# Kernel tuning notes

Hardware: AMD Instinct MI355X
Metric: run time of the kernel (lower is better)

The kernel has to match this reference:

```python
import jax, jax.numpy as jnp
import numpy as np

B, L, D, H = 4, 1024, 1024, 16
HD = D // H          # head dim = 64
NUM_CASES = 8        # Sanskrit vibhakti cases
SCALE = float(np.sqrt(HD))


def setup_inputs() -> dict:
    key = jax.random.key(0)
    ks = jax.random.split(key, 13)
    s = 0.02
    return {
        "x": jax.random.normal(ks[0], (B, L, D), jnp.float32),
        "case_ids": jax.random.randint(ks[1], (B, L), 0, NUM_CASES, jnp.int32),
        "verb_mask": jax.random.randint(ks[2], (B, L), 0, 2, jnp.int32),
        "Wq": jax.random.normal(ks[3], (D, D), jnp.float32) * s,
        "bq": jnp.zeros((D,), jnp.float32),
        "Wk": jax.random.normal(ks[4], (D, D), jnp.float32) * s,
        "bk": jnp.zeros((D,), jnp.float32),
        "Wv": jax.random.normal(ks[5], (D, D), jnp.float32) * s,
        "bv": jnp.zeros((D,), jnp.float32),
        "Wo": jax.random.normal(ks[6], (D, D), jnp.float32) * s,
        "bo": jnp.zeros((D,), jnp.float32),
        "case_bias": jax.random.normal(ks[7], (H, NUM_CASES, NUM_CASES), jnp.float32) * s,
        "verb_bias": jax.random.normal(ks[8], (H,), jnp.float32) * s,
    }


def reference(x, case_ids, verb_mask, Wq, bq, Wk, bk, Wv, bv, Wo, bo, case_bias, verb_bias):
    b, l, d = x.shape

    def split_heads(t):  # [B,L,D] -> [B,H,L,HD]
        return t.reshape(b, l, H, HD).transpose(0, 2, 1, 3)

    Q = split_heads(x @ Wq + bq)
    K = split_heads(x @ Wk + bk)
    V = split_heads(x @ Wv + bv)

    scores = jnp.einsum('bhid,bhjd->bhij', Q, K) / SCALE  # [B,H,L,L]

    # Panini constraint bias: per-head case-pair bias + per-head verb-position bias
    cb = case_bias[:, case_ids[:, :, None], case_ids[:, None, :]]  # [H,B,L,L]
    cb = cb.transpose(1, 0, 2, 3)                                  # [B,H,L,L]
    vb = verb_bias[None, :, None, None] * verb_mask[:, None, None, :].astype(scores.dtype)
    scores = scores + cb + vb

    weights = jax.nn.softmax(scores, axis=-1)  # dropout is identity in eval
    out = jnp.einsum('bhij,bhjd->bhid', weights, V)       # [B,H,L,HD]
    out = out.transpose(0, 2, 1, 3).reshape(b, l, d)
    return out @ Wo + bo
```

## Files before the change

kernel.cpp:

```cpp
#include <hip/hip_runtime.h>

#define BB 4
#define LL 1024
#define DD 1024
#define HH 16
#define HDD 64

typedef __bf16 bf16x8 __attribute__((ext_vector_type(8)));
typedef float f32x4 __attribute__((ext_vector_type(4)));
typedef float f32x16 __attribute__((ext_vector_type(16)));
typedef unsigned short u16x8 __attribute__((ext_vector_type(8)));
typedef unsigned short u16x4 __attribute__((ext_vector_type(4)));
typedef unsigned int u32x4v __attribute__((ext_vector_type(4)));
typedef unsigned int u32x2 __attribute__((ext_vector_type(2)));

#define LOG2E 1.4426950408889634f

__device__ __forceinline__ unsigned short f2bf(float f) {
    unsigned int u = __builtin_bit_cast(unsigned int, f);
    u += 0x7FFFu + ((u >> 16) & 1u);
    return (unsigned short)(u >> 16);
}

__device__ __forceinline__ unsigned int cvtpk_bf16(float lo, float hi) {
    unsigned int r;
    asm("v_cvt_pk_bf16_f32 %0, %1, %2" : "=v"(r) : "v"(lo), "v"(hi));
    return r;
}

__global__ __launch_bounds__(256) void cvt_x(const float* __restrict__ x,
                                             unsigned short* __restrict__ xb) {
    const int i = (blockIdx.x * 256 + threadIdx.x) * 8;
    f32x4 a0 = *(const f32x4*)(x + i);
    f32x4 a1 = *(const f32x4*)(x + i + 4);
    u16x8 o;
#pragma unroll
    for (int j = 0; j < 4; ++j) { o[j] = f2bf(a0[j]); o[4 + j] = f2bf(a1[j]); }
    *(u16x8*)(xb + i) = o;
}

__global__ __launch_bounds__(256) void trans_w(const float* __restrict__ Wq,
                                               const float* __restrict__ Wk,
                                               const float* __restrict__ Wv,
                                               const float* __restrict__ Wo,
                                               unsigned short* __restrict__ Wqkv_t,
                                               unsigned short* __restrict__ Wo_t) {
    __shared__ unsigned short lds[64 * 72];
    const int t = threadIdx.x;
    const int mat = blockIdx.z;
    const float* W = (mat == 0) ? Wq : (mat == 1) ? Wk : (mat == 2) ? Wv : Wo;
    unsigned short* out = (mat < 3) ? (Wqkv_t + (size_t)mat * 1024 * 1024) : Wo_t;
    const int k0 = blockIdx.x * 64;
    const int n0 = blockIdx.y * 64;
#pragma unroll
    for (int p = 0; p < 4; ++p) {
        int c = t + p * 256;
        int kr = c >> 4, c4 = (c & 15) * 4;
        f32x4 v = *(const f32x4*)(W + (size_t)(k0 + kr) * 1024 + n0 + c4);
#pragma unroll
        for (int i = 0; i < 4; ++i) lds[(c4 + i) * 72 + kr] = f2bf(v[i]);
    }
    __syncthreads();
#pragma unroll
    for (int p = 0; p < 2; ++p) {
        int c = t + p * 256;
        int nr = c >> 3, koff = (c & 7) * 8;
        u16x8 vv = *(const u16x8*)&lds[nr * 72 + koff];
        *(u16x8*)(out + (size_t)(n0 + nr) * 1024 + k0 + koff) = vv;
    }
}

__global__ __launch_bounds__(256) void bias_prep(const int* __restrict__ cid,
                                                 const int* __restrict__ vmask,
                                                 const float* __restrict__ case_bias,
                                                 const float* __restrict__ verb_bias,
                                                 float* __restrict__ btab) {
    const int bh = blockIdx.x;
    const int b = bh >> 4, h = bh & 15;
    const float vbh = verb_bias[h] * LOG2E;
    const int t = threadIdx.x;
#pragma unroll
    for (int p = 0; p < 4; ++p) {
        const int j = t + p * 256;
        const int cj = cid[b * LL + j];
        const float vb = vmask[b * LL + j] ? vbh : 0.f;
#pragma unroll
        for (int ci = 0; ci < 8; ++ci)
            btab[((size_t)bh * 8 + ci) * LL + j] = case_bias[h * 64 + ci * 8 + cj] * LOG2E + vb;
    }
}

__global__ __launch_bounds__(256) void gemm_qkv(const unsigned short* __restrict__ Abf,
                                                const unsigned short* __restrict__ Btw,
                                                const float* __restrict__ bq,
                                                const float* __restrict__ bk,
                                                const float* __restrict__ bv,
                                                unsigned short* __restrict__ qkv) {
    __shared__ unsigned short Asm[128 * 32];
    __shared__ unsigned short Bsm[128 * 32];
    const int t = threadIdx.x;
    const int w = t >> 6, lane = t & 63;
    const int wm = w >> 1, wn = w & 1;
    const int lr = lane & 15, lk = (lane >> 4) * 8;
    const int row0 = blockIdx.x * 128;
    const int col0 = blockIdx.y * 128;
    const int r = t >> 2;
    const int cb8 = (t & 3) * 8;

    f32x4 acc[4][4];
#pragma unroll
    for (int mf = 0; mf < 4; ++mf)
#pragma unroll
        for (int nf = 0; nf < 4; ++nf)
#pragma unroll
            for (int e = 0; e < 4; ++e) acc[mf][nf][e] = 0.f;

    for (int kt = 0; kt < 32; ++kt) {
        __syncthreads();
        const int k0 = kt * 32;
#pragma unroll
        for (int p = 0; p < 2; ++p) {
            const unsigned short* sa = Abf + (size_t)(row0 + p * 64 + r) * 1024 + k0 + cb8;
            __builtin_amdgcn_global_load_lds(
                (const __attribute__((address_space(1))) unsigned int*)sa,
                (__attribute__((address_space(3))) unsigned int*)(Asm + p * 2048 + t * 8), 16, 0, 0);
            const unsigned short* sb = Btw + (size_t)(col0 + p * 64 + r) * 1024 + k0 + cb8;
            __builtin_amdgcn_global_load_lds(
                (const __attribute__((address_space(1))) unsigned int*)sb,
                (__attribute__((address_space(3))) unsigned int*)(Bsm + p * 2048 + t * 8), 16, 0, 0);
        }
        __syncthreads();
        bf16x8 af[4], bfr[4];
#pragma unroll
        for (int mf = 0; mf < 4; ++mf)
            af[mf] = *(const bf16x8*)&Asm[(wm * 64 + mf * 16 + lr) * 32 + lk];
#pragma unroll
        for (int nf = 0; nf < 4; ++nf)
            bfr[nf] = *(const bf16x8*)&Bsm[(wn * 64 + nf * 16 + lr) * 32 + lk];
#pragma unroll
        for (int mf = 0; mf < 4; ++mf)
#pragma unroll
            for (int nf = 0; nf < 4; ++nf)
                acc[mf][nf] = __builtin_amdgcn_mfma_f32_16x16x32_bf16(af[mf], bfr[nf], acc[mf][nf], 0, 0, 0);
    }

#pragma unroll
    for (int mf = 0; mf < 4; ++mf) {
        const int grow = row0 + wm * 64 + mf * 16 + (lane >> 4) * 4;
#pragma unroll
        for (int nf = 0; nf < 4; ++nf) {
            const int gcol = col0 + wn * 64 + nf * 16 + lr;
            const int mat = gcol >> 10;
            const int nc_ = gcol & 1023;
            const float bias = (mat == 0) ? bq[nc_] : (mat == 1 ? bk[nc_] : bv[nc_]);
            const float scale = (mat == 0) ? 0.125f * LOG2E : 1.0f;
            const int hh = nc_ >> 6, hd = nc_ & 63;
#pragma unroll
            for (int rr = 0; rr < 4; ++rr) {
                const int row = grow + rr;
                const int bb = row >> 10, ll = row & 1023;
                const float vout = (acc[mf][nf][rr] + bias) * scale;
                qkv[((((size_t)mat * BB + bb) * HH + hh) * LL + ll) * HDD + hd] = f2bf(vout);
            }
        }
    }
}

__global__ __launch_bounds__(256) void vtrans(const unsigned short* __restrict__ Vg,
                                              unsigned short* __restrict__ Vt) {
    __shared__ unsigned short lds[64 * 72];
    const int t = threadIdx.x;
    const int bh = blockIdx.y;
    const int j0 = blockIdx.x * 64;
    const size_t hoff = (size_t)bh * LL * HDD;
#pragma unroll
    for (int p = 0; p < 2; ++p) {
        int c = t + p * 256;
        int jr = c >> 3, doff = (c & 7) * 8;
        u16x8 v = *(const u16x8*)(Vg + hoff + (size_t)(j0 + jr) * 64 + doff);
#pragma unroll
        for (int i = 0; i < 8; ++i) lds[(doff + i) * 72 + jr] = v[i];
    }
    __syncthreads();
#pragma unroll
    for (int p = 0; p < 2; ++p) {
        int c = t + p * 256;
        int dr = c >> 3, joff = (c & 7) * 8;
        u16x8 vv = *(const u16x8*)&lds[dr * 72 + joff];
        *(u16x8*)(Vt + hoff + (size_t)dr * 1024 + j0 + joff) = vv;
    }
}

__global__ __launch_bounds__(256, 2) void attn8(const unsigned short* __restrict__ Qg,
                                                const unsigned short* __restrict__ Kg,
                                                const unsigned short* __restrict__ Vtg,
                                                const int* __restrict__ cid,
                                                const float* __restrict__ btab,
                                                unsigned short* __restrict__ att) {
    __shared__ unsigned short kvbuf[3 * 8192];
    __shared__ unsigned short tblb[8 * 1056];

    const int t = threadIdx.x;
    const int w = t >> 6;
    const int lane = t & 63;
    const int q31 = lane & 31;
    const int g = lane >> 5;

    const int f = blockIdx.x;
    const int qt = (f >> 3) & 7;
    const int bh = ((f & 7) << 3) | (f >> 6);
    const int b = bh >> 4, h = bh & 15;
    const size_t headoff = (size_t)bh * LL * HDD;
    const int q0 = qt * 128;
    const int qrow = q0 + w * 32 + q31;

    bf16x8 qf[4];
    {
        const unsigned short* qp = Qg + headoff + (size_t)qrow * HDD + g * 8;
        qf[0] = *(const bf16x8*)(qp);
        qf[1] = *(const bf16x8*)(qp + 16);
        qf[2] = *(const bf16x8*)(qp + 32);
        qf[3] = *(const bf16x8*)(qp + 48);
    }
    const int ci = cid[b * LL + qrow];
    const int tb_lane = ci * 1060 + 4 * g;

    const int r8 = lane >> 3, c8 = lane & 7;

#define STAGE(base_sh, j0s)                                                                        \
    {                                                                                              \
        _Pragma("unroll") for (int cc = 0; cc < 2; ++cc) {                                         \
            const int chunk = w + cc * 4;                                                          \
            const int row = chunk * 8 + r8;                                                        \
            const int sc8 = (c8 ^ (row & 7)) * 8;                                                  \
            const unsigned short* srck = Kg + headoff + (size_t)((j0s) + row) * HDD + sc8;         \
            __builtin_amdgcn_global_load_lds(                                                      \
                (const __attribute__((address_space(1))) unsigned int*)srck,                       \
                (__attribute__((address_space(3))) unsigned int*)(&kvbuf[(base_sh) + chunk * 512]),\
                16, 0, 0);                                                                         \
            const unsigned short* srcv = Vtg + headoff + (size_t)row * LL + (j0s) + sc8;           \
            __builtin_amdgcn_global_load_lds(                                                      \
                (const __attribute__((address_space(1))) unsigned int*)srcv,                       \
                (__attribute__((address_space(3))) unsigned int*)(&kvbuf[(base_sh) + 4096 +        \
                                                                         chunk * 512]),           \
                16, 0, 0);                                                                         \
        }                                                                                          \
    }

    STAGE(0, 0);
    STAGE(8192, 64);
    for (int e = t; e < 8192; e += 256) {
        const int cie = e >> 10, j = e & 1023;
        tblb[cie * 1060 + j] = f2bf(btab[(size_t)bh * 8192 + e]);
    }
    __syncthreads();

    f32x16 acc0, acc1, sum16;
#pragma unroll
    for (int e = 0; e < 16; ++e) { acc0[e] = 0.f; acc1[e] = 0.f; sum16[e] = 0.f; }

    int cur = 0, stg = 2;
    for (int jt = 0; jt < 16; ++jt) {
        if (jt == 15) asm volatile("s_waitcnt vmcnt(0)" ::: "memory");
        else          asm volatile("s_waitcnt vmcnt(4)" ::: "memory");
        __builtin_amdgcn_s_barrier();
        asm volatile("" ::: "memory");

        if (jt < 14) STAGE(stg * 8192, (jt + 2) * 64);

        const unsigned short* kvb = &kvbuf[cur * 8192];

        f32x16 st[2];
#pragma unroll
        for (int jt2 = 0; jt2 < 2; ++jt2) {
            f32x16 s;
#pragma unroll
            for (int q = 0; q < 4; ++q) {
                const u32x2 bw = *(const u32x2*)&tblb[tb_lane + jt * 64 + jt2 * 32 + 8 * q];
                s[4 * q + 0] = __builtin_bit_cast(float, bw[0] << 16);
                s[4 * q + 1] = __builtin_bit_cast(float, bw[0] & 0xFFFF0000u);
                s[4 * q + 2] = __builtin_bit_cast(float, bw[1] << 16);
                s[4 * q + 3] = __builtin_bit_cast(float, bw[1] & 0xFFFF0000u);
            }
            const int arow = jt2 * 32 + q31;
            const unsigned short* kb = &kvb[arow * 64];
            const int swz = arow & 7;
            __builtin_amdgcn_s_setprio(1);
#pragma unroll
            for (int kk = 0; kk < 4; ++kk) {
                bf16x8 af = *(const bf16x8*)&kb[((2 * kk + g) ^ swz) * 8];
                s = __builtin_amdgcn_mfma_f32_32x32x16_bf16(af, qf[kk], s, 0, 0, 0);
            }
            __builtin_amdgcn_s_setprio(0);
            st[jt2] = s;
        }

#pragma unroll
        for (int jt2 = 0; jt2 < 2; ++jt2)
#pragma unroll
            for (int r = 0; r < 16; ++r) {
                const float p = __builtin_amdgcn_exp2f(st[jt2][r]);
                st[jt2][r] = p;
                sum16[r] += p;
            }

        __builtin_amdgcn_s_setprio(1);
#pragma unroll
        for (int kk = 0; kk < 4; ++kk) {
            const int jt2 = kk >> 1, rb = (kk & 1) * 8;
            unsigned int a0 = cvtpk_bf16(st[jt2][rb + 0], st[jt2][rb + 1]);
            unsigned int b0 = cvtpk_bf16(st[jt2][rb + 4], st[jt2][rb + 5]);
            unsigned int a1 = cvtpk_bf16(st[jt2][rb + 2], st[jt2][rb + 3]);
            unsigned int b1 = cvtpk_bf16(st[jt2][rb + 6], st[jt2][rb + 7]);
            u32x2 r0 = __builtin_amdgcn_permlane32_swap(a0, b0, false, false);
            u32x2 r1 = __builtin_amdgcn_permlane32_swap(a1, b1, false, false);
            u32x4v pw;
            pw[0] = r0[0]; pw[1] = r1[0]; pw[2] = r0[1]; pw[3] = r1[1];
            const bf16x8 pf = __builtin_bit_cast(bf16x8, pw);
#pragma unroll
            for (int dt = 0; dt < 2; ++dt) {
                const int vrow = dt * 32 + q31;
                const bf16x8 vf =
                    *(const bf16x8*)&kvb[4096 + vrow * 64 + (((2 * kk + g) ^ (vrow & 7)) * 8)];
                if (dt == 0)
                    acc0 = __builtin_amdgcn_mfma_f32_32x32x16_bf16(vf, pf, acc0, 0, 0, 0);
                else
                    acc1 = __builtin_amdgcn_mfma_f32_32x32x16_bf16(vf, pf, acc1, 0, 0, 0);
            }
        }
        __builtin_amdgcn_s_setprio(0);

        cur = (cur == 2) ? 0 : cur + 1;
        stg = (stg == 2) ? 0 : stg + 1;
    }
#undef STAGE

    float l_run = 0.f;
#pragma unroll
    for (int e = 0; e < 16; ++e) l_run += sum16[e];
    l_run += __shfl_xor(l_run, 32);

    __syncthreads();
    const float inv = 1.0f / l_run;
    unsigned short* ob = &kvbuf[0];
    const int orow = w * 32 + q31;
    const int oswz = (orow & 7) << 3;
#pragma unroll
    for (int dt = 0; dt < 2; ++dt) {
#pragma unroll
        for (int u = 0; u < 4; ++u) {
            u16x4 v4;
#pragma unroll
            for (int v = 0; v < 4; ++v)
                v4[v] = f2bf((dt ? acc1[4 * u + v] : acc0[4 * u + v]) * inv);
            const int d0 = dt * 32 + 8 * u + 4 * g;
            *(u16x4*)&ob[orow * 64 + (d0 ^ oswz)] = v4;
        }
    }
    __syncthreads();
#pragma unroll
    for (int p = 0; p < 4; ++p) {
        const int row = p * 32 + (t >> 3);
        const int c16 = t & 7;
        u16x8 v = *(const u16x8*)&ob[row * 64 + ((c16 ^ (row & 7)) * 8)];
        *(u16x8*)(att + (size_t)(b * LL + q0 + row) * DD + h * 64 + c16 * 8) = v;
    }
}

__global__ __launch_bounds__(256) void gemm_out(const unsigned short* __restrict__ Abf,
                                                const unsigned short* __restrict__ Btw,
                                                const float* __restrict__ bo,
                                                float* __restrict__ out) {
    __shared__ unsigned short Asm[128 * 32];
    __shared__ unsigned short Bsm[128 * 32];
    const int t = threadIdx.x;
    const int w = t >> 6, lane = t & 63;
    const int wm = w >> 1, wn = w & 1;
    const int lr = lane & 15, lk = (lane >> 4) * 8;
    const int row0 = blockIdx.x * 128;
    const int col0 = blockIdx.y * 128;
    const int r = t >> 2;
    const int cb8 = (t & 3) * 8;

    f32x4 acc[4][4];
#pragma unroll
    for (int mf = 0; mf < 4; ++mf)
#pragma unroll
        for (int nf = 0; nf < 4; ++nf)
#pragma unroll
            for (int e = 0; e < 4; ++e) acc[mf][nf][e] = 0.f;

    for (int kt = 0; kt < 32; ++kt) {
        __syncthreads();
        const int k0 = kt * 32;
#pragma unroll
        for (int p = 0; p < 2; ++p) {
            const unsigned short* sa = Abf + (size_t)(row0 + p * 64 + r) * 1024 + k0 + cb8;
            __builtin_amdgcn_global_load_lds(
                (const __attribute__((address_space(1))) unsigned int*)sa,
                (__attribute__((address_space(3))) unsigned int*)(Asm + p * 2048 + t * 8), 16, 0, 0);
            const unsigned short* sb = Btw + (size_t)(col0 + p * 64 + r) * 1024 + k0 + cb8;
            __builtin_amdgcn_global_load_lds(
                (const __attribute__((address_space(1))) unsigned int*)sb,
                (__attribute__((address_space(3))) unsigned int*)(Bsm + p * 2048 + t * 8), 16, 0, 0);
        }
        __syncthreads();
        bf16x8 af[4], bfr[4];
#pragma unroll
        for (int mf = 0; mf < 4; ++mf)
            af[mf] = *(const bf16x8*)&Asm[(wm * 64 + mf * 16 + lr) * 32 + lk];
#pragma unroll
        for (int nf = 0; nf < 4; ++nf)
            bfr[nf] = *(const bf16x8*)&Bsm[(wn * 64 + nf * 16 + lr) * 32 + lk];
#pragma unroll
        for (int mf = 0; mf < 4; ++mf)
#pragma unroll
            for (int nf = 0; nf < 4; ++nf)
                acc[mf][nf] = __builtin_amdgcn_mfma_f32_16x16x32_bf16(af[mf], bfr[nf], acc[mf][nf], 0, 0, 0);
    }

#pragma unroll
    for (int mf = 0; mf < 4; ++mf) {
        const int grow = row0 + wm * 64 + mf * 16 + (lane >> 4) * 4;
#pragma unroll
        for (int nf = 0; nf < 4; ++nf) {
            const int gcol = col0 + wn * 64 + nf * 16 + lr;
            const float bias = bo[gcol];
#pragma unroll
            for (int rr = 0; rr < 4; ++rr)
                out[(size_t)(grow + rr) * 1024 + gcol] = acc[mf][nf][rr] + bias;
        }
    }
}

extern "C" void kernel_launch(void* const* d_in, const int* in_sizes, int n_in,
                              void* d_out, int out_size, void* d_ws, size_t ws_size,
                              hipStream_t stream) {
    const float* x = (const float*)d_in[0];
    const int* cid = (const int*)d_in[1];
    const int* vmask = (const int*)d_in[2];
    const float* Wq = (const float*)d_in[3];
    const float* bq = (const float*)d_in[4];
    const float* Wk = (const float*)d_in[5];
    const float* bk = (const float*)d_in[6];
    const float* Wv = (const float*)d_in[7];
    const float* bv = (const float*)d_in[8];
    const float* Wo = (const float*)d_in[9];
    const float* bo = (const float*)d_in[10];
    const float* case_bias = (const float*)d_in[11];
    const float* verb_bias = (const float*)d_in[12];
    float* out = (float*)d_out;

    char* ws = (char*)d_ws;
    unsigned short* xb     = (unsigned short*)(ws);
    unsigned short* Wqkv_t = (unsigned short*)(ws + ((size_t)8 << 20));
    unsigned short* Wo_t   = (unsigned short*)(ws + ((size_t)14 << 20));
    unsigned short* qkv    = (unsigned short*)(ws + ((size_t)16 << 20));
    unsigned short* Vt     = (unsigned short*)(ws + ((size_t)40 << 20));
    unsigned short* att    = (unsigned short*)(ws + ((size_t)48 << 20));
    float*          btab   = (float*)(ws + ((size_t)56 << 20));

    const size_t MATSZ = (size_t)BB * HH * LL * HDD;

    hipLaunchKernelGGL(cvt_x, dim3(2048), dim3(256), 0, stream, x, xb);
    hipLaunchKernelGGL(trans_w, dim3(16, 16, 4), dim3(256), 0, stream, Wq, Wk, Wv, Wo, Wqkv_t, Wo_t);
    hipLaunchKernelGGL(bias_prep, dim3(64), dim3(256), 0, stream, cid, vmask, case_bias, verb_bias, btab);
    hipLaunchKernelGGL(gemm_qkv, dim3(32, 24), dim3(256), 0, stream, xb, Wqkv_t, bq, bk, bv, qkv);
    hipLaunchKernelGGL(vtrans, dim3(16, 64), dim3(256), 0, stream, qkv + 2 * MATSZ, Vt);
    hipLaunchKernelGGL(attn8, dim3(512), dim3(256), 0, stream,
                       qkv, qkv + MATSZ, Vt, cid, btab, att);
    hipLaunchKernelGGL(gemm_out, dim3(32, 8), dim3(256), 0, stream, att, Wo_t, bo, out);
}
```

Before: 103.8 us.

## Software-pipeline attention loop: overlap next tile's QK with current softmax and PV

Restructures the attention main loop into a two-stage software pipeline, unrolled by two with ping-pong score registers. The QK^T MFMAs for tile j+1 are issued before the exp and PV MFMAs of tile j, so matrix-core work can overlap the exp/convert VALU work. The cost is two extra 16-float score vectors per thread, which raises register pressure at two waves per SIMD. The wait also tightens from vmcnt(4) to vmcnt(0), giving up some load/compute overlap in the triple-buffered staging.

```diff
diff --git a/kernel.cpp b/kernel.cpp
--- a/kernel.cpp
+++ b/kernel.cpp
@@ -191,7 +191,81 @@
     }
 }
 
-__global__ __launch_bounds__(256, 2) void attn8(const unsigned short* __restrict__ Qg,
+__device__ __forceinline__ void qk64(f32x16& s0, f32x16& s1, const unsigned short* kvb,
+                                     const unsigned short* tbl, const bf16x8 (&qf)[4],
+                                     int q31, int g) {
+#pragma unroll
+    for (int jt2 = 0; jt2 < 2; ++jt2) {
+        f32x16 s;
+#pragma unroll
+        for (int q = 0; q < 4; ++q) {
+            const u32x2 bw = *(const u32x2*)&tbl[jt2 * 32 + 8 * q];
+            s[4 * q + 0] = __builtin_bit_cast(float, bw[0] << 16);
+            s[4 * q + 1] = __builtin_bit_cast(float, bw[0] & 0xFFFF0000u);
+            s[4 * q + 2] = __builtin_bit_cast(float, bw[1] << 16);
+            s[4 * q + 3] = __builtin_bit_cast(float, bw[1] & 0xFFFF0000u);
+        }
+        const int arow = jt2 * 32 + q31;
+        const unsigned short* kb = &kvb[arow * 64];
+        const int swz = arow & 7;
+        __builtin_amdgcn_s_setprio(1);
+#pragma unroll
+        for (int kk = 0; kk < 4; ++kk) {
+            bf16x8 af = *(const bf16x8*)&kb[((2 * kk + g) ^ swz) * 8];
+            s = __builtin_amdgcn_mfma_f32_32x32x16_bf16(af, qf[kk], s, 0, 0, 0);
+        }
+        __builtin_amdgcn_s_setprio(0);
+        if (jt2 == 0) s0 = s; else s1 = s;
+    }
+}
+
+__device__ __forceinline__ void sm64(f32x16& s0, f32x16& s1, f32x16& sum16) {
+#pragma unroll
+    for (int r = 0; r < 16; ++r) {
+        const float p = __builtin_amdgcn_exp2f(s0[r]);
+        s0[r] = p;
+        sum16[r] += p;
+    }
+#pragma unroll
+    for (int r = 0; r < 16; ++r) {
+        const float p = __builtin_amdgcn_exp2f(s1[r]);
+        s1[r] = p;
+        sum16[r] += p;
+    }
+}
+
+__device__ __forceinline__ void pv64(const f32x16& s0, const f32x16& s1,
+                                     const unsigned short* kvb, int q31, int g,
+                                     f32x16& acc0, f32x16& acc1) {
+    __builtin_amdgcn_s_setprio(1);
+#pragma unroll
+    for (int kk = 0; kk < 4; ++kk) {
+        const f32x16& sj = (kk & 2) ? s1 : s0;
+        const int rb = (kk & 1) * 8;
+        unsigned int a0 = cvtpk_bf16(sj[rb + 0], sj[rb + 1]);
+        unsigned int b0 = cvtpk_bf16(sj[rb + 4], sj[rb + 5]);
+        unsigned int a1 = cvtpk_bf16(sj[rb + 2], sj[rb + 3]);
+        unsigned int b1 = cvtpk_bf16(sj[rb + 6], sj[rb + 7]);
+        u32x2 r0 = __builtin_amdgcn_permlane32_swap(a0, b0, false, false);
+        u32x2 r1 = __builtin_amdgcn_permlane32_swap(a1, b1, false, false);
+        u32x4v pw;
+        pw[0] = r0[0]; pw[1] = r1[0]; pw[2] = r0[1]; pw[3] = r1[1];
+        const bf16x8 pf = __builtin_bit_cast(bf16x8, pw);
+#pragma unroll
+        for (int dt = 0; dt < 2; ++dt) {
+            const int vrow = dt * 32 + q31;
+            const bf16x8 vf =
+                *(const bf16x8*)&kvb[4096 + vrow * 64 + (((2 * kk + g) ^ (vrow & 7)) * 8)];
+            if (dt == 0)
+                acc0 = __builtin_amdgcn_mfma_f32_32x32x16_bf16(vf, pf, acc0, 0, 0, 0);
+            else
+                acc1 = __builtin_amdgcn_mfma_f32_32x32x16_bf16(vf, pf, acc1, 0, 0, 0);
+        }
+    }
+    __builtin_amdgcn_s_setprio(0);
+}
+
+__global__ __launch_bounds__(256, 2) void attn9(const unsigned short* __restrict__ Qg,
                                                 const unsigned short* __restrict__ Kg,
                                                 const unsigned short* __restrict__ Vtg,
                                                 const int* __restrict__ cid,
@@ -259,79 +333,30 @@
 #pragma unroll
     for (int e = 0; e < 16; ++e) { acc0[e] = 0.f; acc1[e] = 0.f; sum16[e] = 0.f; }
 
-    int cur = 0, stg = 2;
-    for (int jt = 0; jt < 16; ++jt) {
-        if (jt == 15) asm volatile("s_waitcnt vmcnt(0)" ::: "memory");
-        else          asm volatile("s_waitcnt vmcnt(4)" ::: "memory");
+    f32x16 sA0, sA1, sB0, sB1;
+    int curo = 0, nxto = 8192, stgo = 16384;
+
+    qk64(sA0, sA1, &kvbuf[0], &tblb[tb_lane], qf, q31, g);
+
+    for (int jt = 0; jt < 16; jt += 2) {
+        asm volatile("s_waitcnt vmcnt(0)" ::: "memory");
         __builtin_amdgcn_s_barrier();
         asm volatile("" ::: "memory");
-
-        if (jt < 14) STAGE(stg * 8192, (jt + 2) * 64);
-
-        const unsigned short* kvb = &kvbuf[cur * 8192];
-
-        f32x16 st[2];
-#pragma unroll
-        for (int jt2 = 0; jt2 < 2; ++jt2) {
-            f32x16 s;
-#pragma unroll
-            for (int q = 0; q < 4; ++q) {
-                const u32x2 bw = *(const u32x2*)&tblb[tb_lane + jt * 64 + jt2 * 32 + 8 * q];
-                s[4 * q + 0] = __builtin_bit_cast(float, bw[0] << 16);
-                s[4 * q + 1] = __builtin_bit_cast(float, bw[0] & 0xFFFF0000u);
-                s[4 * q + 2] = __builtin_bit_cast(float, bw[1] << 16);
-                s[4 * q + 3] = __builtin_bit_cast(float, bw[1] & 0xFFFF0000u);
-            }
-            const int arow = jt2 * 32 + q31;
-            const unsigned short* kb = &kvb[arow * 64];
-            const int swz = arow & 7;
-            __builtin_amdgcn_s_setprio(1);
-#pragma unroll
-            for (int kk = 0; kk < 4; ++kk) {
-                bf16x8 af = *(const bf16x8*)&kb[((2 * kk + g) ^ swz) * 8];
-                s = __builtin_amdgcn_mfma_f32_32x32x16_bf16(af, qf[kk], s, 0, 0, 0);
-            }
-            __builtin_amdgcn_s_setprio(0);
-            st[jt2] = s;
-        }
-
-#pragma unroll
-        for (int jt2 = 0; jt2 < 2; ++jt2)
-#pragma unroll
-            for (int r = 0; r < 16; ++r) {
-                const float p = __builtin_amdgcn_exp2f(st[jt2][r]);
-                st[jt2][r] = p;
-                sum16[r] += p;
-            }
-
-        __builtin_amdgcn_s_setprio(1);
-#pragma unroll
-        for (int kk = 0; kk < 4; ++kk) {
-            const int jt2 = kk >> 1, rb = (kk & 1) * 8;
-            unsigned int a0 = cvtpk_bf16(st[jt2][rb + 0], st[jt2][rb + 1]);
-            unsigned int b0 = cvtpk_bf16(st[jt2][rb + 4], st[jt2][rb + 5]);
-            unsigned int a1 = cvtpk_bf16(st[jt2][rb + 2], st[jt2][rb + 3]);
-            unsigned int b1 = cvtpk_bf16(st[jt2][rb + 6], st[jt2][rb + 7]);
-            u32x2 r0 = __builtin_amdgcn_permlane32_swap(a0, b0, false, false);
-            u32x2 r1 = __builtin_amdgcn_permlane32_swap(a1, b1, false, false);
-            u32x4v pw;
-            pw[0] = r0[0]; pw[1] = r1[0]; pw[2] = r0[1]; pw[3] = r1[1];
-            const bf16x8 pf = __builtin_bit_cast(bf16x8, pw);
-#pragma unroll
-            for (int dt = 0; dt < 2; ++dt) {
-                const int vrow = dt * 32 + q31;
-                const bf16x8 vf =
-                    *(const bf16x8*)&kvb[4096 + vrow * 64 + (((2 * kk + g) ^ (vrow & 7)) * 8)];
-                if (dt == 0)
-                    acc0 = __builtin_amdgcn_mfma_f32_32x32x16_bf16(vf, pf, acc0, 0, 0, 0);
-                else
-                    acc1 = __builtin_amdgcn_mfma_f32_32x32x16_bf16(vf, pf, acc1, 0, 0, 0);
-            }
-        }
-        __builtin_amdgcn_s_setprio(0);
-
-        cur = (cur == 2) ? 0 : cur + 1;
-        stg = (stg == 2) ? 0 : stg + 1;
+        if (jt + 2 < 16) STAGE(stgo, (jt + 2) * 64);
+        qk64(sB0, sB1, &kvbuf[nxto], &tblb[tb_lane + (jt + 1) * 64], qf, q31, g);
+        sm64(sA0, sA1, sum16);
+        pv64(sA0, sA1, &kvbuf[curo], q31, g, acc0, acc1);
+        { int tmp = curo; curo = nxto; nxto = stgo; stgo = tmp; }
+
+        asm volatile("s_waitcnt vmcnt(0)" ::: "memory");
+        __builtin_amdgcn_s_barrier();
+        asm volatile("" ::: "memory");
+        if (jt + 3 < 16) STAGE(stgo, (jt + 3) * 64);
+        if (jt + 2 < 16)
+            qk64(sA0, sA1, &kvbuf[nxto], &tblb[tb_lane + (jt + 2) * 64], qf, q31, g);
+        sm64(sB0, sB1, sum16);
+        pv64(sB0, sB1, &kvbuf[curo], q31, g, acc0, acc1);
+        { int tmp = curo; curo = nxto; nxto = stgo; stgo = tmp; }
     }
 #undef STAGE
 
@@ -467,7 +492,7 @@
     hipLaunchKernelGGL(bias_prep, dim3(64), dim3(256), 0, stream, cid, vmask, case_bias, verb_bias, btab);
     hipLaunchKernelGGL(gemm_qkv, dim3(32, 24), dim3(256), 0, stream, xb, Wqkv_t, bq, bk, bv, qkv);
     hipLaunchKernelGGL(vtrans, dim3(16, 64), dim3(256), 0, stream, qkv + 2 * MATSZ, Vt);
-    hipLaunchKernelGGL(attn8, dim3(512), dim3(256), 0, stream,
+    hipLaunchKernelGGL(attn9, dim3(512), dim3(256), 0, stream,
                        qkv, qkv + MATSZ, Vt, cid, btab, att);
     hipLaunchKernelGGL(gemm_out, dim3(32, 8), dim3(256), 0, stream, att, Wo_t, bo, out);
 }
```

Result: no change. 103.9 us (+0.1%).

## Give each attention wave private K/V double buffers and drop block barriers

Applied to the files above, without the earlier changes.

The attention kernel now has each wave stream its own 32-key K/V tiles into a private double-buffered LDS region, so the block-wide barriers are gone. The bias table is re-laid out in MFMA output order in fp32 and read straight from global memory into registers, which removes the bf16 LDS table staging. Each wave reloads the same K/V tiles that the other waves also load, so global/L2 traffic rises fourfold. Waiting on vmcnt(0) each step also limits prefetch depth to one tile.

```diff
diff --git a/kernel.cpp b/kernel.cpp
--- a/kernel.cpp
+++ b/kernel.cpp
@@ -70,23 +70,23 @@
     }
 }
 
-__global__ __launch_bounds__(256) void bias_prep(const int* __restrict__ cid,
-                                                 const int* __restrict__ vmask,
-                                                 const float* __restrict__ case_bias,
-                                                 const float* __restrict__ verb_bias,
-                                                 float* __restrict__ btab) {
+__global__ __launch_bounds__(256) void bias_prep3(const int* __restrict__ cid,
+                                                  const int* __restrict__ vmask,
+                                                  const float* __restrict__ case_bias,
+                                                  const float* __restrict__ verb_bias,
+                                                  float* __restrict__ btab3) {
     const int bh = blockIdx.x;
     const int b = bh >> 4, h = bh & 15;
     const float vbh = verb_bias[h] * LOG2E;
-    const int t = threadIdx.x;
-#pragma unroll
-    for (int p = 0; p < 4; ++p) {
-        const int j = t + p * 256;
+    for (int idx = threadIdx.x; idx < 8192; idx += 256) {
+        const int ci = idx >> 10;
+        const int g = (idx >> 9) & 1;
+        const int pos = idx & 511;
+        const int tg = pos >> 4, r = pos & 15;
+        const int j = tg * 32 + (r & 3) + 8 * (r >> 2) + 4 * g;
         const int cj = cid[b * LL + j];
         const float vb = vmask[b * LL + j] ? vbh : 0.f;
-#pragma unroll
-        for (int ci = 0; ci < 8; ++ci)
-            btab[((size_t)bh * 8 + ci) * LL + j] = case_bias[h * 64 + ci * 8 + cj] * LOG2E + vb;
+        btab3[(size_t)bh * 8192 + idx] = case_bias[h * 64 + ci * 8 + cj] * LOG2E + vb;
     }
 }
 
@@ -191,20 +191,70 @@
     }
 }
 
-__global__ __launch_bounds__(256, 2) void attn8(const unsigned short* __restrict__ Qg,
-                                                const unsigned short* __restrict__ Kg,
-                                                const unsigned short* __restrict__ Vtg,
-                                                const int* __restrict__ cid,
-                                                const float* __restrict__ btab,
-                                                unsigned short* __restrict__ att) {
-    __shared__ unsigned short kvbuf[3 * 8192];
-    __shared__ unsigned short tblb[8 * 1056];
+__device__ __forceinline__ void ctile32(const unsigned short* kb, const f32x4 (&bb)[4],
+                                        const bf16x8 (&qf)[4], int q31, int g,
+                                        f32x16& acc0, f32x16& acc1, f32x16& sum16) {
+    f32x16 s;
+#pragma unroll
+    for (int r = 0; r < 16; ++r) s[r] = bb[r >> 2][r & 3];
+    const int swz = q31 & 7;
+    __builtin_amdgcn_s_setprio(1);
+#pragma unroll
+    for (int kk = 0; kk < 4; ++kk) {
+        const bf16x8 af = *(const bf16x8*)&kb[q31 * 64 + (((2 * kk + g) ^ swz) * 8)];
+        s = __builtin_amdgcn_mfma_f32_32x32x16_bf16(af, qf[kk], s, 0, 0, 0);
+    }
+    __builtin_amdgcn_s_setprio(0);
+
+#pragma unroll
+    for (int r = 0; r < 16; ++r) {
+        const float p = __builtin_amdgcn_exp2f(s[r]);
+        s[r] = p;
+        sum16[r] += p;
+    }
+
+    __builtin_amdgcn_s_setprio(1);
+#pragma unroll
+    for (int ks = 0; ks < 2; ++ks) {
+        const int rb = ks * 8;
+        unsigned int a0 = cvtpk_bf16(s[rb + 0], s[rb + 1]);
+        unsigned int b0 = cvtpk_bf16(s[rb + 4], s[rb + 5]);
+        unsigned int a1 = cvtpk_bf16(s[rb + 2], s[rb + 3]);
+        unsigned int b1 = cvtpk_bf16(s[rb + 6], s[rb + 7]);
+        u32x2 r0 = __builtin_amdgcn_permlane32_swap(a0, b0, false, false);
+        u32x2 r1 = __builtin_amdgcn_permlane32_swap(a1, b1, false, false);
+        u32x4v pw;
+        pw[0] = r0[0]; pw[1] = r1[0]; pw[2] = r0[1]; pw[3] = r1[1];
+        const bf16x8 pf = __builtin_bit_cast(bf16x8, pw);
+#pragma unroll
+        for (int dt = 0; dt < 2; ++dt) {
+            const int vrow = dt * 32 + q31;
+            const bf16x8 vf =
+                *(const bf16x8*)&kb[2048 + vrow * 32 + (((2 * ks + g) ^ ((vrow >> 1) & 3)) * 8)];
+            if (dt == 0)
+                acc0 = __builtin_amdgcn_mfma_f32_32x32x16_bf16(vf, pf, acc0, 0, 0, 0);
+            else
+                acc1 = __builtin_amdgcn_mfma_f32_32x32x16_bf16(vf, pf, acc1, 0, 0, 0);
+        }
+    }
+    __builtin_amdgcn_s_setprio(0);
+}
+
+__global__ __launch_bounds__(256, 2) void attn10(const unsigned short* __restrict__ Qg,
+                                                 const unsigned short* __restrict__ Kg,
+                                                 const unsigned short* __restrict__ Vtg,
+                                                 const int* __restrict__ cid,
+                                                 const float* __restrict__ btab3,
+                                                 unsigned short* __restrict__ att) {
+    __shared__ unsigned short kvbuf[4][8192];
 
     const int t = threadIdx.x;
     const int w = t >> 6;
     const int lane = t & 63;
     const int q31 = lane & 31;
     const int g = lane >> 5;
+    const int r8 = lane >> 3, c8 = lane & 7;
+    const int r4 = lane >> 2, c4 = lane & 3;
 
     const int f = blockIdx.x;
     const int qt = (f >> 3) & 7;
@@ -223,115 +273,56 @@
         qf[3] = *(const bf16x8*)(qp + 48);
     }
     const int ci = cid[b * LL + qrow];
-    const int tb_lane = ci * 1060 + 4 * g;
-
-    const int r8 = lane >> 3, c8 = lane & 7;
-
-#define STAGE(base_sh, j0s)                                                                        \
+    const float* bbase = btab3 + ((size_t)(bh * 8 + ci) * 2 + g) * 512;
+
+    unsigned short* kpriv = &kvbuf[w][0];
+
+#define STAGE(boff, j0s)                                                                           \
     {                                                                                              \
-        _Pragma("unroll") for (int cc = 0; cc < 2; ++cc) {                                         \
-            const int chunk = w + cc * 4;                                                          \
-            const int row = chunk * 8 + r8;                                                        \
-            const int sc8 = (c8 ^ (row & 7)) * 8;                                                  \
-            const unsigned short* srck = Kg + headoff + (size_t)((j0s) + row) * HDD + sc8;         \
+        _Pragma("unroll") for (int cc = 0; cc < 4; ++cc) {                                         \
+            const int rowk = cc * 8 + r8;                                                          \
+            const unsigned short* srck =                                                           \
+                Kg + headoff + (size_t)((j0s) + rowk) * HDD + ((c8 ^ (rowk & 7)) * 8);             \
             __builtin_amdgcn_global_load_lds(                                                      \
                 (const __attribute__((address_space(1))) unsigned int*)srck,                       \
-                (__attribute__((address_space(3))) unsigned int*)(&kvbuf[(base_sh) + chunk * 512]),\
-                16, 0, 0);                                                                         \
-            const unsigned short* srcv = Vtg + headoff + (size_t)row * LL + (j0s) + sc8;           \
+                (__attribute__((address_space(3))) unsigned int*)(kpriv + (boff) + cc * 512), 16,  \
+                0, 0);                                                                             \
+            const int dv = cc * 16 + r4;                                                           \
+            const unsigned short* srcv =                                                           \
+                Vtg + headoff + (size_t)dv * LL + (j0s) + ((c4 ^ ((dv >> 1) & 3)) * 8);            \
             __builtin_amdgcn_global_load_lds(                                                      \
                 (const __attribute__((address_space(1))) unsigned int*)srcv,                       \
-                (__attribute__((address_space(3))) unsigned int*)(&kvbuf[(base_sh) + 4096 +        \
-                                                                         chunk * 512]),           \
+                (__attribute__((address_space(3))) unsigned int*)(kpriv + (boff) + 2048 +          \
+                                                                  cc * 512),                      \
                 16, 0, 0);                                                                         \
         }                                                                                          \
     }
 
+    f32x16 acc0, acc1, sum16;
+#pragma unroll
+    for (int e = 0; e < 16; ++e) { acc0[e] = 0.f; acc1[e] = 0.f; sum16[e] = 0.f; }
+
+    f32x4 bA[4], bB[4];
     STAGE(0, 0);
-    STAGE(8192, 64);
-    for (int e = t; e < 8192; e += 256) {
-        const int cie = e >> 10, j = e & 1023;
-        tblb[cie * 1060 + j] = f2bf(btab[(size_t)bh * 8192 + e]);
-    }
-    __syncthreads();
-
-    f32x16 acc0, acc1, sum16;
-#pragma unroll
-    for (int e = 0; e < 16; ++e) { acc0[e] = 0.f; acc1[e] = 0.f; sum16[e] = 0.f; }
-
-    int cur = 0, stg = 2;
-    for (int jt = 0; jt < 16; ++jt) {
-        if (jt == 15) asm volatile("s_waitcnt vmcnt(0)" ::: "memory");
-        else          asm volatile("s_waitcnt vmcnt(4)" ::: "memory");
-        __builtin_amdgcn_s_barrier();
-        asm volatile("" ::: "memory");
-
-        if (jt < 14) STAGE(stg * 8192, (jt + 2) * 64);
-
-        const unsigned short* kvb = &kvbuf[cur * 8192];
-
-        f32x16 st[2];
-#pragma unroll
-        for (int jt2 = 0; jt2 < 2; ++jt2) {
-            f32x16 s;
-#pragma unroll
-            for (int q = 0; q < 4; ++q) {
-                const u32x2 bw = *(const u32x2*)&tblb[tb_lane + jt * 64 + jt2 * 32 + 8 * q];
-                s[4 * q + 0] = __builtin_bit_cast(float, bw[0] << 16);
-                s[4 * q + 1] = __builtin_bit_cast(float, bw[0] & 0xFFFF0000u);
-                s[4 * q + 2] = __builtin_bit_cast(float, bw[1] << 16);
-                s[4 * q + 3] = __builtin_bit_cast(float, bw[1] & 0xFFFF0000u);
-            }
-            const int arow = jt2 * 32 + q31;
-            const unsigned short* kb = &kvb[arow * 64];
-            const int swz = arow & 7;
-            __builtin_amdgcn_s_setprio(1);
-#pragma unroll
-            for (int kk = 0; kk < 4; ++kk) {
-                bf16x8 af = *(const bf16x8*)&kb[((2 * kk + g) ^ swz) * 8];
-                s = __builtin_amdgcn_mfma_f32_32x32x16_bf16(af, qf[kk], s, 0, 0, 0);
-            }
-            __builtin_amdgcn_s_setprio(0);
-            st[jt2] = s;
-        }
-
-#pragma unroll
-        for (int jt2 = 0; jt2 < 2; ++jt2)
-#pragma unroll
-            for (int r = 0; r < 16; ++r) {
-                const float p = __builtin_amdgcn_exp2f(st[jt2][r]);
-                st[jt2][r] = p;
-                sum16[r] += p;
-            }
-
-        __builtin_amdgcn_s_setprio(1);
-#pragma unroll
-        for (int kk = 0; kk < 4; ++kk) {
-            const int jt2 = kk >> 1, rb = (kk & 1) * 8;
-            unsigned int a0 = cvtpk_bf16(st[jt2][rb + 0], st[jt2][rb + 1]);
-            unsigned int b0 = cvtpk_bf16(st[jt2][rb + 4], st[jt2][rb + 5]);
-            unsigned int a1 = cvtpk_bf16(st[jt2][rb + 2], st[jt2][rb + 3]);
-            unsigned int b1 = cvtpk_bf16(st[jt2][rb + 6], st[jt2][rb + 7]);
-            u32x2 r0 = __builtin_amdgcn_permlane32_swap(a0, b0, false, false);
-            u32x2 r1 = __builtin_amdgcn_permlane32_swap(a1, b1, false, false);
-            u32x4v pw;
-            pw[0] = r0[0]; pw[1] = r1[0]; pw[2] = r0[1]; pw[3] = r1[1];
-            const bf16x8 pf = __builtin_bit_cast(bf16x8, pw);
-#pragma unroll
-            for (int dt = 0; dt < 2; ++dt) {
-                const int vrow = dt * 32 + q31;
-                const bf16x8 vf =
-                    *(const bf16x8*)&kvb[4096 + vrow * 64 + (((2 * kk + g) ^ (vrow & 7)) * 8)];
-                if (dt == 0)
-                    acc0 = __builtin_amdgcn_mfma_f32_32x32x16_bf16(vf, pf, acc0, 0, 0, 0);
-                else
-                    acc1 = __builtin_amdgcn_mfma_f32_32x32x16_bf16(vf, pf, acc1, 0, 0, 0);
-            }
-        }
-        __builtin_amdgcn_s_setprio(0);
-
-        cur = (cur == 2) ? 0 : cur + 1;
-        stg = (stg == 2) ? 0 : stg + 1;
+#pragma unroll
+    for (int i = 0; i < 4; ++i) bA[i] = *(const f32x4*)(bbase + 4 * i);
+
+    for (int jt = 0; jt < 32; jt += 2) {
+        asm volatile("s_waitcnt vmcnt(0)" ::: "memory");
+        if (jt + 1 < 32) {
+            STAGE(4096, (jt + 1) * 32);
+#pragma unroll
+            for (int i = 0; i < 4; ++i) bB[i] = *(const f32x4*)(bbase + (jt + 1) * 16 + 4 * i);
+        }
+        ctile32(kpriv, bA, qf, q31, g, acc0, acc1, sum16);
+
+        asm volatile("s_waitcnt vmcnt(0)" ::: "memory");
+        if (jt + 2 < 32) {
+            STAGE(0, (jt + 2) * 32);
+#pragma unroll
+            for (int i = 0; i < 4; ++i) bA[i] = *(const f32x4*)(bbase + (jt + 2) * 16 + 4 * i);
+        }
+        ctile32(kpriv + 4096, bB, qf, q31, g, acc0, acc1, sum16);
     }
 #undef STAGE
 
@@ -339,12 +330,10 @@
 #pragma unroll
     for (int e = 0; e < 16; ++e) l_run += sum16[e];
     l_run += __shfl_xor(l_run, 32);
-
-    __syncthreads();
     const float inv = 1.0f / l_run;
-    unsigned short* ob = &kvbuf[0];
-    const int orow = w * 32 + q31;
-    const int oswz = (orow & 7) << 3;
+
+    unsigned short* ob = kpriv;
+    const int oswz = (q31 & 7) << 3;
 #pragma unroll
     for (int dt = 0; dt < 2; ++dt) {
 #pragma unroll
@@ -354,16 +343,14 @@
             for (int v = 0; v < 4; ++v)
                 v4[v] = f2bf((dt ? acc1[4 * u + v] : acc0[4 * u + v]) * inv);
             const int d0 = dt * 32 + 8 * u + 4 * g;
-            *(u16x4*)&ob[orow * 64 + (d0 ^ oswz)] = v4;
-        }
-    }
-    __syncthreads();
+            *(u16x4*)&ob[q31 * 64 + (d0 ^ oswz)] = v4;
+        }
+    }
 #pragma unroll
     for (int p = 0; p < 4; ++p) {
-        const int row = p * 32 + (t >> 3);
-        const int c16 = t & 7;
-        u16x8 v = *(const u16x8*)&ob[row * 64 + ((c16 ^ (row & 7)) * 8)];
-        *(u16x8*)(att + (size_t)(b * LL + q0 + row) * DD + h * 64 + c16 * 8) = v;
+        const int row = p * 8 + r8;
+        u16x8 v = *(const u16x8*)&ob[row * 64 + ((c8 ^ (row & 7)) * 8)];
+        *(u16x8*)(att + (size_t)(b * LL + q0 + w * 32 + row) * DD + h * 64 + c8 * 8) = v;
     }
 }
 
@@ -458,16 +445,16 @@
     unsigned short* qkv    = (unsigned short*)(ws + ((size_t)16 << 20));
     unsigned short* Vt     = (unsigned short*)(ws + ((size_t)40 << 20));
     unsigned short* att    = (unsigned short*)(ws + ((size_t)48 << 20));
-    float*          btab   = (float*)(ws + ((size_t)56 << 20));
+    float*          btab3  = (float*)(ws + ((size_t)56 << 20));
 
     const size_t MATSZ = (size_t)BB * HH * LL * HDD;
 
     hipLaunchKernelGGL(cvt_x, dim3(2048), dim3(256), 0, stream, x, xb);
     hipLaunchKernelGGL(trans_w, dim3(16, 16, 4), dim3(256), 0, stream, Wq, Wk, Wv, Wo, Wqkv_t, Wo_t);
-    hipLaunchKernelGGL(bias_prep, dim3(64), dim3(256), 0, stream, cid, vmask, case_bias, verb_bias, btab);
+    hipLaunchKernelGGL(bias_prep3, dim3(64), dim3(256), 0, stream, cid, vmask, case_bias, verb_bias, btab3);
     hipLaunchKernelGGL(gemm_qkv, dim3(32, 24), dim3(256), 0, stream, xb, Wqkv_t, bq, bk, bv, qkv);
     hipLaunchKernelGGL(vtrans, dim3(16, 64), dim3(256), 0, stream, qkv + 2 * MATSZ, Vt);
-    hipLaunchKernelGGL(attn8, dim3(512), dim3(256), 0, stream,
-                       qkv, qkv + MATSZ, Vt, cid, btab, att);
+    hipLaunchKernelGGL(attn10, dim3(512), dim3(256), 0, stream,
+                       qkv, qkv + MATSZ, Vt, cid, btab3, att);
     hipLaunchKernelGGL(gemm_out, dim3(32, 8), dim3(256), 0, stream, att, Wo_t, bo, out);
 }
```

After: 124.3 us. +19.8%, slower.
